# Optimization experiments

Hardware: AMD Instinct MI355X
Metric: run time of the kernel (lower is better)

The kernel has to match this reference:

```python
import jax, jax.numpy as jnp
import numpy as np

CHNN = 1024
K = 2048


def _conv1x1(W, b, x):
    # x: (B, C_in, L), W: (C_out, C_in), b: (C_out,)
    return jnp.einsum('oc,bcl->bol', W, x) + b[None, :, None]


def setup_inputs() -> dict:
    key = jax.random.key(0)
    ks = jax.random.split(key, 10)
    s = 0.02
    return {
        'vc': jax.random.normal(ks[0], (1, CHNN, K), dtype=jnp.float32),
        'vm': jax.random.normal(ks[1], (1, CHNN, K), dtype=jnp.float32),
        'W_ak': jax.random.normal(ks[2], (K, CHNN), dtype=jnp.float32) * s,
        'b_ak': jax.random.normal(ks[3], (K,), dtype=jnp.float32) * s,
        'W_c': jax.random.normal(ks[4], (CHNN, CHNN), dtype=jnp.float32) * s,
        'b_c': jax.random.normal(ks[5], (CHNN,), dtype=jnp.float32) * s,
        'W_mad': jax.random.normal(ks[6], (CHNN, CHNN), dtype=jnp.float32) * s,
        'b_mad': jax.random.normal(ks[7], (CHNN,), dtype=jnp.float32) * s,
        'W_gcn': jax.random.normal(ks[8], (CHNN, CHNN), dtype=jnp.float32) * s,
        'b_gcn': jax.random.normal(ks[9], (CHNN,), dtype=jnp.float32) * s,
    }


def reference(vc, vm, W_ak, b_ak, W_c, b_c, W_mad, b_mad, W_gcn, b_gcn):
    # vcw: (1, K, L) assignment logits; softmax over the K (channel) dim
    vcw = _conv1x1(W_ak, b_ak, vc)
    vcw = jax.nn.softmax(vcw, axis=1)
    w = vcw[0].T                      # (L, K)  (batch forced to 1 by squeeze(0))
    # vm features: (1, CHNN, K)
    vmr = jax.nn.relu(_conv1x1(W_c, b_c, vm))
    # F.linear(vm, w): contract last dim (K) with w's second dim -> (1, CHNN, L)
    vma = jnp.einsum('bck,lk->bcl', vmr, w)
    vma = _conv1x1(W_mad, b_mad, vma)  # (1, CHNN, L)
    # dense adjacency over positions: (1, L, L)
    A = jnp.einsum('bck,bcl->bkl', vma, vma)
    # GCN: x (1, K, CHNN) @ W + b, then softmax(A) @ x  (requires L == K)
    x = jnp.swapaxes(vmr, 1, 2) @ W_gcn + b_gcn
    A = jax.nn.softmax(A, axis=-1)
    out = A @ x                        # (1, L, CHNN)
    return jnp.swapaxes(out, 1, 2)     # (1, CHNN, L)
```

## Files before the change

kernel.cpp:

```cpp
#include <hip/hip_runtime.h>
#include <hip/hip_bf16.h>


typedef __bf16 bf16x4 __attribute__((ext_vector_type(4)));
typedef __bf16 bf16x8 __attribute__((ext_vector_type(8)));
typedef float  f32x4  __attribute__((ext_vector_type(4)));

typedef const void __attribute__((address_space(1)))* gptr_t;
typedef void       __attribute__((address_space(3)))* lptr_t;

__device__ __forceinline__ void load16_lds(const __bf16* g, __bf16* l)
{
    __builtin_amdgcn_global_load_lds((gptr_t)g, (lptr_t)l, 16, 0, 0);
}

#define WAITCNT_VM16 0x4F70
#define WAITCNT_VM8  0x0F78
#define WAITCNT_VM0  0x0F70

template<typename OT, int BIAS_, bool RELU_, int STORE_>
struct GC {
    using OUT_T = OT;
    static constexpr int BIAS = BIAS_, STORE = STORE_;
    static constexpr bool RELU = RELU_;
};

template<class CF>
__device__ __forceinline__ void gemm_body(
    int bid, __bf16* sA, __bf16* sB,
    const __bf16* __restrict__ A, const __bf16* __restrict__ B,
    const float* __restrict__ bias,
    typename CF::OUT_T* __restrict__ C, typename CF::OUT_T* __restrict__ CT,
    int M, int N, int K, int ntx, bool mirror = false)
{
    const int lane = threadIdx.x & 63;
    const int m0 = (bid / ntx) * 64, n0 = (bid % ntx) * 64;
    const __bf16* gA = A + (size_t)m0 * K;
    const __bf16* gB = B + (size_t)n0 * K;

    f32x4 acc[4][4];
    #pragma unroll
    for (int i = 0; i < 4; ++i)
        #pragma unroll
        for (int j = 0; j < 4; ++j)
            acc[i][j] = (f32x4){0.f, 0.f, 0.f, 0.f};

    auto stage = [&](int k0, int buf) {
        #pragma unroll
        for (int i = 0; i < 4; ++i) {
            const int c = i * 64 + lane;
            const int s = (c ^ (c >> 2) ^ (c >> 4)) & 3;
            load16_lds(gA + (size_t)(c >> 2) * K + k0 + s * 8,
                       &sA[buf * 2048 + i * 512]);
        }
        #pragma unroll
        for (int i = 0; i < 4; ++i) {
            const int c = i * 64 + lane;
            const int s = (c ^ (c >> 2) ^ (c >> 4)) & 3;
            load16_lds(gB + (size_t)(c >> 2) * K + k0 + s * 8,
                       &sB[buf * 2048 + i * 512]);
        }
    };

    const int fsw = ((lane >> 4) ^ lane ^ (lane >> 2)) & 3;

    auto compute = [&](int buf) {
        bf16x8 af[4], bfr[4];
        #pragma unroll
        for (int i = 0; i < 4; ++i) {
            const int off = buf * 2048 + (i * 16 + (lane & 15)) * 32 + fsw * 8;
            af[i]  = *(const bf16x8*)&sA[off];
            bfr[i] = *(const bf16x8*)&sB[off];
        }
        #pragma unroll
        for (int i = 0; i < 4; ++i)
            #pragma unroll
            for (int j = 0; j < 4; ++j)
                acc[i][j] = __builtin_amdgcn_mfma_f32_16x16x32_bf16(af[i], bfr[j], acc[i][j], 0, 0, 0);
    };

    stage(0, 0);
    stage(32, 1);
    stage(64, 2);
    int cur = 0;
    for (int k0 = 0; k0 < K - 96; k0 += 32) {
        __builtin_amdgcn_s_waitcnt(WAITCNT_VM16);
        compute(cur);
        stage(k0 + 96, cur);
        cur = (cur == 2) ? 0 : cur + 1;
    }
    __builtin_amdgcn_s_waitcnt(WAITCNT_VM16);
    compute(cur); cur = (cur == 2) ? 0 : cur + 1;
    __builtin_amdgcn_s_waitcnt(WAITCNT_VM8);
    compute(cur); cur = (cur == 2) ? 0 : cur + 1;
    __builtin_amdgcn_s_waitcnt(WAITCNT_VM0);
    compute(cur);

    #pragma unroll
    for (int i = 0; i < 4; ++i) {
        const int rowb = m0 + i * 16 + (lane >> 4) * 4;
        #pragma unroll
        for (int j = 0; j < 4; ++j) {
            const int col = n0 + j * 16 + (lane & 15);
            f32x4 v = acc[i][j];
            #pragma unroll
            for (int r = 0; r < 4; ++r) {
                float f = v[r];
                if constexpr (CF::BIAS == 1) f += bias[rowb + r];
                if constexpr (CF::BIAS == 2) f += bias[col];
                if constexpr (CF::RELU) f = fmaxf(f, 0.f);
                v[r] = f;
            }
            if constexpr (CF::STORE == 0) {
                #pragma unroll
                for (int r = 0; r < 4; ++r)
                    C[(size_t)(rowb + r) * N + col] = (typename CF::OUT_T)v[r];
                if constexpr (sizeof(typename CF::OUT_T) == 2) {
                    if (mirror) {
                        bf16x4 w = { (__bf16)v[0], (__bf16)v[1],
                                     (__bf16)v[2], (__bf16)v[3] };
                        *(bf16x4*)&C[(size_t)col * N + rowb] = w;
                    }
                }
            } else {
                if constexpr (sizeof(typename CF::OUT_T) == 4) {
                    *(f32x4*)&CT[(size_t)col * M + rowb] = v;
                } else {
                    bf16x4 w = { (__bf16)v[0], (__bf16)v[1], (__bf16)v[2], (__bf16)v[3] };
                    *(bf16x4*)&CT[(size_t)col * M + rowb] = w;
                }
            }
        }
    }
}

__device__ __forceinline__ void softmax_row_w(__bf16* __restrict__ p)
{
    const int lane = threadIdx.x & 63;
    bf16x8 v[4];
    float f[32];
    #pragma unroll
    for (int r = 0; r < 4; ++r)
        v[r] = *(const bf16x8*)&p[(r * 64 + lane) * 8];
    float m = -1e30f;
    #pragma unroll
    for (int r = 0; r < 4; ++r)
        #pragma unroll
        for (int j = 0; j < 8; ++j) {
            f[r * 8 + j] = (float)v[r][j];
            m = fmaxf(m, f[r * 8 + j]);
        }
    #pragma unroll
    for (int s = 1; s < 64; s <<= 1) m = fmaxf(m, __shfl_xor(m, s, 64));
    float sum = 0.f;
    #pragma unroll
    for (int i = 0; i < 32; ++i) { f[i] = expf(f[i] - m); sum += f[i]; }
    #pragma unroll
    for (int s = 1; s < 64; s <<= 1) sum += __shfl_xor(sum, s, 64);
    const float inv = 1.f / sum;
    #pragma unroll
    for (int r = 0; r < 4; ++r) {
        bf16x8 w;
        #pragma unroll
        for (int j = 0; j < 8; ++j) w[j] = (__bf16)(f[r * 8 + j] * inv);
        *(bf16x8*)&p[(r * 64 + lane) * 8] = w;
    }
}

template<class CF>
__global__ __launch_bounds__(64, 2)
void gemm1w(const __bf16* __restrict__ A, const __bf16* __restrict__ B,
            const float* __restrict__ bias,
            typename CF::OUT_T* __restrict__ C, typename CF::OUT_T* __restrict__ CT,
            int M, int N, int K, int ntx)
{
    __shared__ __bf16 sAB[12288];
    gemm_body<CF>(blockIdx.x, sAB, sAB + 4096 + 2048, A, B, bias, C, CT, M, N, K, ntx);
}

template<class CF>
__global__ __launch_bounds__(64, 2)
void gemm1wsym(const __bf16* __restrict__ A,
               typename CF::OUT_T* __restrict__ C,
               int M, int K, int ntx)
{
    __shared__ __bf16 sAB[12288];
    int rem = blockIdx.x, ti = 0, rowlen = ntx;
    while (rem >= rowlen) { rem -= rowlen; ++ti; --rowlen; }
    const int tj = ti + rem;
    gemm_body<CF>(ti * ntx + tj, sAB, sAB + 6144, A, A, nullptr, C,
                  (typename CF::OUT_T*)nullptr, M, M, K, ntx, ti != tj);
}

template<class C1, class C2>
__global__ __launch_bounds__(64, 2)
void gemm2w(int nblk1,
            const __bf16* __restrict__ A1, const __bf16* __restrict__ B1,
            const float* __restrict__ b1,
            typename C1::OUT_T* __restrict__ C1p, typename C1::OUT_T* __restrict__ CT1,
            int M1, int N1, int K1, int ntx1,
            const __bf16* __restrict__ A2, const __bf16* __restrict__ B2,
            const float* __restrict__ b2,
            typename C2::OUT_T* __restrict__ C2p, typename C2::OUT_T* __restrict__ CT2,
            int M2, int N2, int K2, int ntx2)
{
    __shared__ __bf16 sAB[12288];
    const int b = blockIdx.x;
    if (b < nblk1)
        gemm_body<C1>(b, sAB, sAB + 6144, A1, B1, b1, C1p, CT1, M1, N1, K1, ntx1);
    else
        gemm_body<C2>(b - nblk1, sAB, sAB + 6144, A2, B2, b2, C2p, CT2, M2, N2, K2, ntx2);
}

template<class C1, class C2>
__global__ __launch_bounds__(64, 2)
void gemm2smw(int nblk1, int nblk2,
              const __bf16* __restrict__ A1, const __bf16* __restrict__ B1,
              const float* __restrict__ b1, typename C1::OUT_T* __restrict__ C1p,
              int M1, int N1, int K1, int ntx1,
              const __bf16* __restrict__ A2, const __bf16* __restrict__ B2,
              const float* __restrict__ b2, typename C2::OUT_T* __restrict__ C2p,
              int M2, int N2, int K2, int ntx2,
              __bf16* __restrict__ SM)
{
    __shared__ __bf16 sAB[12288];
    const int b = blockIdx.x;
    if (b < nblk1)
        gemm_body<C1>(b, sAB, sAB + 6144, A1, B1, b1, C1p,
                      (typename C1::OUT_T*)nullptr, M1, N1, K1, ntx1);
    else if (b < nblk1 + nblk2)
        gemm_body<C2>(b - nblk1, sAB, sAB + 6144, A2, B2, b2, C2p,
                      (typename C2::OUT_T*)nullptr, M2, N2, K2, ntx2);
    else
        softmax_row_w(SM + (size_t)(b - nblk1 - nblk2) * 2048);
}

__global__ __launch_bounds__(64)
void row_softmax_w(__bf16* __restrict__ A)
{
    softmax_row_w(A + (size_t)blockIdx.x * 2048);
}

__device__ __forceinline__ void tp_tile(const float* __restrict__ in,
                                        __bf16* __restrict__ outp,
                                        int R, int C, int bx, int by)
{
    __shared__ float t[32][33];
    const int tx = threadIdx.x & 31, ty = threadIdx.x >> 5;
    #pragma unroll
    for (int i = ty; i < 32; i += 8)
        t[i][tx] = in[(size_t)(by + i) * C + (bx + tx)];
    __syncthreads();
    #pragma unroll
    for (int i = ty; i < 32; i += 8)
        outp[(size_t)(bx + i) * R + (by + tx)] = (__bf16)t[tx][i];
}

__device__ __forceinline__ void cast_blk(const float* __restrict__ s,
                                         __bf16* __restrict__ d, int blk)
{
    const int i = blk * 1024 + threadIdx.x * 4;
    float4 v = *(const float4*)&s[i];
    bf16x4 w = { (__bf16)v.x, (__bf16)v.y, (__bf16)v.z, (__bf16)v.w };
    *(bf16x4*)&d[i] = w;
}

__global__ __launch_bounds__(256)
void prep(const float* __restrict__ vc, __bf16* __restrict__ vcT,
          const float* __restrict__ vm, __bf16* __restrict__ vmT,
          const float* __restrict__ W_ak, __bf16* __restrict__ W_akb,
          const float* __restrict__ W_c, __bf16* __restrict__ W_cb,
          const float* __restrict__ W_mad, __bf16* __restrict__ W_madb,
          const float* __restrict__ W_gcn, __bf16* __restrict__ W_gcnT)
{
    const int x = blockIdx.x;
    if (blockIdx.z == 0) {
        const float* in = (x < 2048) ? vc : vm;
        __bf16* o       = (x < 2048) ? vcT : vmT;
        const int e = x & 2047;
        tp_tile(in, o, 1024, 2048, (e & 63) * 32, (e >> 6) * 32);
    } else if (blockIdx.z == 1) {
        if (x < 2048)      cast_blk(W_ak, W_akb, x);
        else if (x < 3072) cast_blk(W_c, W_cb, x - 2048);
        else               cast_blk(W_mad, W_madb, x - 3072);
    } else {
        if (x >= 1024) return;
        tp_tile(W_gcn, W_gcnT, 1024, 1024, (x & 31) * 32, (x >> 5) * 32);
    }
}

extern "C" void kernel_launch(void* const* d_in, const int* in_sizes, int n_in,
                              void* d_out, int out_size, void* d_ws, size_t ws_size,
                              hipStream_t stream)
{
    const float* vc    = (const float*)d_in[0];
    const float* vm    = (const float*)d_in[1];
    const float* W_ak  = (const float*)d_in[2];
    const float* b_ak  = (const float*)d_in[3];
    const float* W_c   = (const float*)d_in[4];
    const float* b_c   = (const float*)d_in[5];
    const float* W_mad = (const float*)d_in[6];
    const float* b_mad = (const float*)d_in[7];
    const float* W_gcn = (const float*)d_in[8];
    const float* b_gcn = (const float*)d_in[9];
    float* out = (float*)d_out;

    char* ws = (char*)d_ws;
    const size_t MB = 1u << 20;
    __bf16* ST     = (__bf16*)(ws);
    __bf16* P      = (__bf16*)(ws);
    __bf16* vcT    = (__bf16*)(ws + 8 * MB);
    __bf16* vmaT   = (__bf16*)(ws + 8 * MB);
    __bf16* W_akb  = (__bf16*)(ws + 12 * MB);
    __bf16* vmm    = (__bf16*)(ws + 12 * MB);
    __bf16* vmT    = (__bf16*)(ws + 16 * MB);
    __bf16* xT     = (__bf16*)(ws + 16 * MB);
    __bf16* W_cb   = (__bf16*)(ws + 20 * MB);
    __bf16* W_madb = (__bf16*)(ws + 22 * MB);
    __bf16* vmrT   = (__bf16*)(ws + 24 * MB);
    __bf16* W_gcnT = (__bf16*)(ws + 28 * MB);

    using G3  = GC<__bf16, 2, false, 0>;
    using G5  = GC<__bf16, 1, true,  1>;
    using G6  = GC<__bf16, 0, false, 0>;
    using G11 = GC<__bf16, 1, false, 0>;
    using G7  = GC<__bf16, 2, false, 0>;
    using G9  = GC<__bf16, 0, false, 0>;
    using G12 = GC<float,  0, false, 1>;

    prep<<<dim3(4096, 1, 3), 256, 0, stream>>>(vc, vcT, vm, vmT, W_ak, W_akb,
                                               W_c, W_cb, W_mad, W_madb,
                                               W_gcn, W_gcnT);
    gemm2w<G3, G5><<<1536, 64, 0, stream>>>(1024,
        vcT, W_akb, b_ak, ST, (__bf16*)nullptr, 2048, 2048, 1024, 32,
        W_cb, vmT, b_c, (__bf16*)nullptr, vmrT, 1024, 2048, 1024, 32);
    gemm2smw<G6, G11><<<3072, 64, 0, stream>>>(512, 512,
        W_madb, vmrT, nullptr, vmm, 1024, 2048, 1024, 32,
        W_gcnT, vmrT, b_gcn, xT, 1024, 2048, 1024, 32,
        ST);
    gemm1w<G7><<<512, 64, 0, stream>>>(ST, vmm, b_mad, vmaT, (__bf16*)nullptr,
                                       2048, 1024, 2048, 16);
    gemm1wsym<G9><<<528, 64, 0, stream>>>(vmaT, P, 2048, 1024, 32);
    row_softmax_w<<<2048, 64, 0, stream>>>(P);
    gemm1w<G12><<<512, 64, 0, stream>>>(P, xT, nullptr, (float*)nullptr, out,
                                        2048, 1024, 2048, 16);
}
```

Before: 198.1 us.

## Use 64x128 single-wave GEMM tiles with triple-buffered LDS pipeline

Adds a new GEMM body that computes a 64x128 output tile per single-wave block, where the old body computed a smaller tile. The new body uses a three-stage global-to-LDS prefetch ring with matching waitcnt thresholds. It is applied to all non-symmetric GEMM launches, halving their grid sizes, and the launch bounds and LDS allocation change to match. The goal is more data reuse per loaded fragment and deeper latency hiding. The cost is larger accumulator register use, lower occupancy and fewer blocks to spread across the CUs.

```diff
diff --git a/kernel.cpp b/kernel.cpp
--- a/kernel.cpp
+++ b/kernel.cpp
@@ -14,7 +14,9 @@
     __builtin_amdgcn_global_load_lds((gptr_t)g, (lptr_t)l, 16, 0, 0);
 }
 
+#define WAITCNT_VM24 0x4F78
 #define WAITCNT_VM16 0x4F70
+#define WAITCNT_VM12 0x0F7C
 #define WAITCNT_VM8  0x0F78
 #define WAITCNT_VM0  0x0F70
 
@@ -134,6 +136,122 @@
     }
 }
 
+template<class CF>
+__device__ __forceinline__ void gemm_body2(
+    int bid, __bf16* sA, __bf16* sB,
+    const __bf16* __restrict__ A, const __bf16* __restrict__ B,
+    const float* __restrict__ bias,
+    typename CF::OUT_T* __restrict__ C, typename CF::OUT_T* __restrict__ CT,
+    int M, int N, int K, int ntx)
+{
+    const int lane = threadIdx.x & 63;
+    const int m0 = (bid / ntx) * 64, n0 = (bid % ntx) * 128;
+    const __bf16* gA = A + (size_t)m0 * K;
+    const __bf16* gB = B + (size_t)n0 * K;
+
+    f32x4 acc[2][4][4];
+    #pragma unroll
+    for (int h = 0; h < 2; ++h)
+        #pragma unroll
+        for (int i = 0; i < 4; ++i)
+            #pragma unroll
+            for (int j = 0; j < 4; ++j)
+                acc[h][i][j] = (f32x4){0.f, 0.f, 0.f, 0.f};
+
+    auto stage = [&](int k0, int buf) {
+        #pragma unroll
+        for (int i = 0; i < 4; ++i) {
+            const int c = i * 64 + lane;
+            const int s = (c ^ (c >> 2) ^ (c >> 4)) & 3;
+            load16_lds(gA + (size_t)(c >> 2) * K + k0 + s * 8,
+                       &sA[buf * 2048 + i * 512]);
+        }
+        #pragma unroll
+        for (int i = 0; i < 8; ++i) {
+            const int c = i * 64 + lane;
+            const int s = (c ^ (c >> 2) ^ (c >> 4)) & 3;
+            load16_lds(gB + (size_t)(c >> 2) * K + k0 + s * 8,
+                       &sB[buf * 4096 + i * 512]);
+        }
+    };
+
+    auto compute = [&](int buf) {
+        bf16x8 af[4];
+        #pragma unroll
+        for (int i = 0; i < 4; ++i) {
+            const int ra = i * 16 + (lane & 15);
+            const int sa = ((lane >> 4) ^ ra ^ (ra >> 2)) & 3;
+            af[i] = *(const bf16x8*)&sA[buf * 2048 + ra * 32 + sa * 8];
+        }
+        #pragma unroll
+        for (int h = 0; h < 2; ++h) {
+            bf16x8 bfr[4];
+            #pragma unroll
+            for (int j = 0; j < 4; ++j) {
+                const int rb = h * 64 + j * 16 + (lane & 15);
+                const int sb = ((lane >> 4) ^ rb ^ (rb >> 2)) & 3;
+                bfr[j] = *(const bf16x8*)&sB[buf * 4096 + rb * 32 + sb * 8];
+            }
+            #pragma unroll
+            for (int i = 0; i < 4; ++i)
+                #pragma unroll
+                for (int j = 0; j < 4; ++j)
+                    acc[h][i][j] = __builtin_amdgcn_mfma_f32_16x16x32_bf16(
+                        af[i], bfr[j], acc[h][i][j], 0, 0, 0);
+        }
+    };
+
+    stage(0, 0);
+    stage(32, 1);
+    stage(64, 2);
+    int cur = 0;
+    for (int k0 = 0; k0 < K - 96; k0 += 32) {
+        __builtin_amdgcn_s_waitcnt(WAITCNT_VM24);
+        compute(cur);
+        stage(k0 + 96, cur);
+        cur = (cur == 2) ? 0 : cur + 1;
+    }
+    __builtin_amdgcn_s_waitcnt(WAITCNT_VM24);
+    compute(cur); cur = (cur == 2) ? 0 : cur + 1;
+    __builtin_amdgcn_s_waitcnt(WAITCNT_VM12);
+    compute(cur); cur = (cur == 2) ? 0 : cur + 1;
+    __builtin_amdgcn_s_waitcnt(WAITCNT_VM0);
+    compute(cur);
+
+    #pragma unroll
+    for (int h = 0; h < 2; ++h) {
+        #pragma unroll
+        for (int i = 0; i < 4; ++i) {
+            const int rowb = m0 + i * 16 + (lane >> 4) * 4;
+            #pragma unroll
+            for (int j = 0; j < 4; ++j) {
+                const int col = n0 + h * 64 + j * 16 + (lane & 15);
+                f32x4 v = acc[h][i][j];
+                #pragma unroll
+                for (int r = 0; r < 4; ++r) {
+                    float f = v[r];
+                    if constexpr (CF::BIAS == 1) f += bias[rowb + r];
+                    if constexpr (CF::BIAS == 2) f += bias[col];
+                    if constexpr (CF::RELU) f = fmaxf(f, 0.f);
+                    v[r] = f;
+                }
+                if constexpr (CF::STORE == 0) {
+                    #pragma unroll
+                    for (int r = 0; r < 4; ++r)
+                        C[(size_t)(rowb + r) * N + col] = (typename CF::OUT_T)v[r];
+                } else {
+                    if constexpr (sizeof(typename CF::OUT_T) == 4) {
+                        *(f32x4*)&CT[(size_t)col * M + rowb] = v;
+                    } else {
+                        bf16x4 w = { (__bf16)v[0], (__bf16)v[1], (__bf16)v[2], (__bf16)v[3] };
+                        *(bf16x4*)&CT[(size_t)col * M + rowb] = w;
+                    }
+                }
+            }
+        }
+    }
+}
+
 __device__ __forceinline__ void softmax_row_w(__bf16* __restrict__ p)
 {
     const int lane = threadIdx.x & 63;
@@ -168,14 +286,14 @@
 }
 
 template<class CF>
-__global__ __launch_bounds__(64, 2)
+__global__ __launch_bounds__(64, 1)
 void gemm1w(const __bf16* __restrict__ A, const __bf16* __restrict__ B,
             const float* __restrict__ bias,
             typename CF::OUT_T* __restrict__ C, typename CF::OUT_T* __restrict__ CT,
             int M, int N, int K, int ntx)
 {
-    __shared__ __bf16 sAB[12288];
-    gemm_body<CF>(blockIdx.x, sAB, sAB + 4096 + 2048, A, B, bias, C, CT, M, N, K, ntx);
+    __shared__ __bf16 sAB[18432];
+    gemm_body2<CF>(blockIdx.x, sAB, sAB + 6144, A, B, bias, C, CT, M, N, K, ntx);
 }
 
 template<class CF>
@@ -193,7 +311,7 @@
 }
 
 template<class C1, class C2>
-__global__ __launch_bounds__(64, 2)
+__global__ __launch_bounds__(64, 1)
 void gemm2w(int nblk1,
             const __bf16* __restrict__ A1, const __bf16* __restrict__ B1,
             const float* __restrict__ b1,
@@ -204,16 +322,16 @@
             typename C2::OUT_T* __restrict__ C2p, typename C2::OUT_T* __restrict__ CT2,
             int M2, int N2, int K2, int ntx2)
 {
-    __shared__ __bf16 sAB[12288];
+    __shared__ __bf16 sAB[18432];
     const int b = blockIdx.x;
     if (b < nblk1)
-        gemm_body<C1>(b, sAB, sAB + 6144, A1, B1, b1, C1p, CT1, M1, N1, K1, ntx1);
+        gemm_body2<C1>(b, sAB, sAB + 6144, A1, B1, b1, C1p, CT1, M1, N1, K1, ntx1);
     else
-        gemm_body<C2>(b - nblk1, sAB, sAB + 6144, A2, B2, b2, C2p, CT2, M2, N2, K2, ntx2);
+        gemm_body2<C2>(b - nblk1, sAB, sAB + 6144, A2, B2, b2, C2p, CT2, M2, N2, K2, ntx2);
 }
 
 template<class C1, class C2>
-__global__ __launch_bounds__(64, 2)
+__global__ __launch_bounds__(64, 1)
 void gemm2smw(int nblk1, int nblk2,
               const __bf16* __restrict__ A1, const __bf16* __restrict__ B1,
               const float* __restrict__ b1, typename C1::OUT_T* __restrict__ C1p,
@@ -223,14 +341,14 @@
               int M2, int N2, int K2, int ntx2,
               __bf16* __restrict__ SM)
 {
-    __shared__ __bf16 sAB[12288];
+    __shared__ __bf16 sAB[18432];
     const int b = blockIdx.x;
     if (b < nblk1)
-        gemm_body<C1>(b, sAB, sAB + 6144, A1, B1, b1, C1p,
-                      (typename C1::OUT_T*)nullptr, M1, N1, K1, ntx1);
+        gemm_body2<C1>(b, sAB, sAB + 6144, A1, B1, b1, C1p,
+                       (typename C1::OUT_T*)nullptr, M1, N1, K1, ntx1);
     else if (b < nblk1 + nblk2)
-        gemm_body<C2>(b - nblk1, sAB, sAB + 6144, A2, B2, b2, C2p,
-                      (typename C2::OUT_T*)nullptr, M2, N2, K2, ntx2);
+        gemm_body2<C2>(b - nblk1, sAB, sAB + 6144, A2, B2, b2, C2p,
+                       (typename C2::OUT_T*)nullptr, M2, N2, K2, ntx2);
     else
         softmax_row_w(SM + (size_t)(b - nblk1 - nblk2) * 2048);
 }
@@ -331,17 +449,17 @@
     prep<<<dim3(4096, 1, 3), 256, 0, stream>>>(vc, vcT, vm, vmT, W_ak, W_akb,
                                                W_c, W_cb, W_mad, W_madb,
                                                W_gcn, W_gcnT);
-    gemm2w<G3, G5><<<1536, 64, 0, stream>>>(1024,
-        vcT, W_akb, b_ak, ST, (__bf16*)nullptr, 2048, 2048, 1024, 32,
-        W_cb, vmT, b_c, (__bf16*)nullptr, vmrT, 1024, 2048, 1024, 32);
-    gemm2smw<G6, G11><<<3072, 64, 0, stream>>>(512, 512,
-        W_madb, vmrT, nullptr, vmm, 1024, 2048, 1024, 32,
-        W_gcnT, vmrT, b_gcn, xT, 1024, 2048, 1024, 32,
+    gemm2w<G3, G5><<<768, 64, 0, stream>>>(512,
+        vcT, W_akb, b_ak, ST, (__bf16*)nullptr, 2048, 2048, 1024, 16,
+        W_cb, vmT, b_c, (__bf16*)nullptr, vmrT, 1024, 2048, 1024, 16);
+    gemm2smw<G6, G11><<<2560, 64, 0, stream>>>(256, 256,
+        W_madb, vmrT, nullptr, vmm, 1024, 2048, 1024, 16,
+        W_gcnT, vmrT, b_gcn, xT, 1024, 2048, 1024, 16,
         ST);
-    gemm1w<G7><<<512, 64, 0, stream>>>(ST, vmm, b_mad, vmaT, (__bf16*)nullptr,
-                                       2048, 1024, 2048, 16);
+    gemm1w<G7><<<256, 64, 0, stream>>>(ST, vmm, b_mad, vmaT, (__bf16*)nullptr,
+                                       2048, 1024, 2048, 8);
     gemm1wsym<G9><<<528, 64, 0, stream>>>(vmaT, P, 2048, 1024, 32);
     row_softmax_w<<<2048, 64, 0, stream>>>(P);
-    gemm1w<G12><<<512, 64, 0, stream>>>(P, xT, nullptr, (float*)nullptr, out,
-                                        2048, 1024, 2048, 16);
-}
+    gemm1w<G12><<<256, 64, 0, stream>>>(P, xT, nullptr, (float*)nullptr, out,
+                                        2048, 1024, 2048, 8);
+}
```

After: 233.7 us. 18.0% more time.
